# Kernel optimization log

Hardware: AMD Instinct MI355X
Metric: run time of the kernel (lower is better)

Reference implementation:

```python
import jax, jax.numpy as jnp
import numpy as np

NUM_HEADS = 4
C_IN = 80   # in_channels[0] (raw camera BEV channels)
C = 126     # in_channels[1]
D = C + 2   # 128, inner attention dim


def _conv(x, w, b=None):
    # NCHW conv, 3x3, SAME padding (padding=1)
    y = jax.lax.conv_general_dilated(x, w, (1, 1), 'SAME',
                                     dimension_numbers=('NCHW', 'OIHW', 'NCHW'))
    if b is not None:
        y = y + b[None, :, None, None]
    return y


def setup_inputs() -> dict:
    key = jax.random.key(0)
    ks = jax.random.split(key, 16)
    s = 0.02
    inp = {
        'lidar_bev': jax.random.normal(ks[0], (1, C, 64, 64), jnp.float32),
        'cam_bev': jax.random.normal(ks[1], (1, C_IN, 64, 64), jnp.float32),
        'cam_enc_w': jax.random.normal(ks[2], (C, C_IN, 3, 3), jnp.float32) * s,
        'cam_enc_b': jnp.zeros((C,), jnp.float32),
        'cam_v_w': jax.random.normal(ks[3], (D, C), jnp.float32) * s,
        'cam_qk_w': jax.random.normal(ks[4], (2 * D, C), jnp.float32) * s,
        'cam_proj_w': jax.random.normal(ks[5], (C, D), jnp.float32) * s,
        'cam_proj_b': jnp.zeros((C,), jnp.float32),
        'lidar_v_w': jax.random.normal(ks[6], (D, C), jnp.float32) * s,
        'lidar_qk_w': jax.random.normal(ks[7], (2 * D, C), jnp.float32) * s,
        'lidar_proj_w': jax.random.normal(ks[8], (C, D), jnp.float32) * s,
        'lidar_proj_b': jnp.zeros((C,), jnp.float32),
        'fuser_w': jax.random.normal(ks[9], (C, 4 * C, 3, 3), jnp.float32) * s,
    }
    return inp


def reference(lidar_bev, cam_bev, cam_enc_w, cam_enc_b, cam_v_w, cam_qk_w,
              cam_proj_w, cam_proj_b, lidar_v_w, lidar_qk_w, lidar_proj_w,
              lidar_proj_b, fuser_w):
    B, Cc, H, W = lidar_bev.shape
    N = H * W
    nh, hd = NUM_HEADS, D // NUM_HEADS
    scale = Cc ** (-0.5)  # in_channels[1] ** -0.5

    cam_enc = _conv(cam_bev, cam_enc_w, cam_enc_b)  # [B,C,H,W] (SCNET stand-in)

    cam_f = cam_enc.reshape(B, Cc, N).transpose(0, 2, 1)     # [B,N,C]
    lid_f = lidar_bev.reshape(B, Cc, N).transpose(0, 2, 1)    # [B,N,C]

    def heads(x):  # [B,N,D] -> [B,nh,N,hd]
        return x.reshape(B, N, nh, hd).transpose(0, 2, 1, 3)

    cam_v = heads(cam_f @ cam_v_w.T)
    lid_v = heads(lid_f @ lidar_v_w.T)

    def qk(x, w):  # -> (q, k) each [B,nh,N,hd]
        t = (x @ w.T).reshape(B, N, 2, nh, hd).transpose(2, 0, 3, 1, 4)
        return t[0], t[1]

    lid_q, lid_k = qk(lid_f, lidar_qk_w)
    cam_q, cam_k = qk(cam_f, cam_qk_w)

    def merge(o):  # [B,nh,N,hd] -> [B,N,D]
        return o.transpose(0, 2, 1, 3).reshape(B, N, D)

    def to_map(x):  # [B,N,C] -> [B,C,H,W]
        return x.reshape(B, H, W, Cc).transpose(0, 3, 1, 2)

    # lidar-driven attention, reused against two value tensors
    lid_attn = jax.nn.softmax(jnp.einsum('bhnd,bhmd->bhnm', lid_q, lid_k) * scale, axis=-1)
    cam_by_lid = to_map(merge(lid_attn @ cam_v) @ cam_proj_w.T + cam_proj_b)
    cam_bev_l = cam_enc + cam_by_lid
    lid_by_lid = to_map(merge(lid_attn @ lid_v) @ lidar_proj_w.T + lidar_proj_b)
    lidar_bev_l = lidar_bev + lid_by_lid

    # camera-driven attention (note: original code uses lidar_proj for BOTH outputs here)
    cam_attn = jax.nn.softmax(jnp.einsum('bhnd,bhmd->bhnm', cam_q, cam_k) * scale, axis=-1)
    cam_by_cam = to_map(merge(cam_attn @ cam_v) @ lidar_proj_w.T + lidar_proj_b)
    cam_bev_c = cam_enc + cam_by_cam
    lid_by_cam = to_map(merge(cam_attn @ lid_v) @ lidar_proj_w.T + lidar_proj_b)
    lidar_bev_c = lidar_bev + lid_by_cam

    fused_in = jnp.concatenate([cam_bev_c, cam_bev_l, lidar_bev_c, lidar_bev_l], axis=1)
    return _conv(fused_in, fuser_w)
```

## Files before the change

### kernel.cpp

```cpp
#include <hip/hip_runtime.h>
#include <hip/hip_bf16.h>

typedef unsigned short ushort_t;
using f32x4  = __attribute__((ext_vector_type(4))) float;
using bf16x8 = __attribute__((ext_vector_type(8))) short;

#define N_PIX 4096

static __device__ __forceinline__ unsigned short f2bf(float f) {
  unsigned int u = __builtin_bit_cast(unsigned int, f);
  u += 0x7FFFu + ((u >> 16) & 1u);
  return (unsigned short)(u >> 16);
}
static __device__ __forceinline__ float bf2f(unsigned int us) {
  return __builtin_bit_cast(float, us << 16);
}

typedef union {
  uint4 u4;
  unsigned long long q[2];
  bf16x8 v;
  unsigned short us[8];
} fragU;

#define LDS_U32(p) ((unsigned)(uintptr_t)((__attribute__((address_space(3))) void*)(p)))

__global__ __launch_bounds__(256) void zero_span_k(uint4* __restrict__ p, int n16) {
  int i = blockIdx.x * 256 + threadIdx.x;
  if (i < n16) p[i] = (uint4){0u, 0u, 0u, 0u};
}

__global__ __launch_bounds__(256) void pack_w_k(
    const float* __restrict__ cam_enc_w, const float* __restrict__ fuser_w,
    const float* __restrict__ lid_proj_w, const float* __restrict__ cam_proj_w,
    const float* __restrict__ lid_qk_w, const float* __restrict__ cam_qk_w,
    const float* __restrict__ cam_v_w, const float* __restrict__ lid_v_w,
    ushort_t* __restrict__ Wp_c, ushort_t* __restrict__ Wp_f,
    ushort_t* __restrict__ Wp_lid, ushort_t* __restrict__ Wp_cam,
    ushort_t* __restrict__ Wq) {
  const float QSCALE = 0.08908708063747479f * 1.4426950408889634f;
  int idx = blockIdx.x * 256 + threadIdx.x;
  if (idx < 110592) {
    int kk = idx / 12288, r = idx % 12288;
    int co = r / 96, ci = r % 96;
    float v = (co < 126 && ci < 80) ? cam_enc_w[(co * 80 + ci) * 9 + kk] : 0.f;
    Wp_c[idx] = f2bf(v);
  } else if (idx < 700416) {
    int j = idx - 110592;
    int kk = j / 65536, r = j % 65536;
    int co = r / 512, ci = r % 512;
    float v = (co < 126 && ci < 504) ? fuser_w[(co * 504 + ci) * 9 + kk] : 0.f;
    Wp_f[j] = f2bf(v);
  } else if (idx < 716800) {
    int j = idx - 700416;
    int co = j >> 7, k = j & 127;
    Wp_lid[j] = f2bf(co < 126 ? lid_proj_w[co * 128 + k] : 0.f);
  } else if (idx < 733184) {
    int j = idx - 716800;
    int co = j >> 7, k = j & 127;
    Wp_cam[j] = f2bf(co < 126 ? cam_proj_w[co * 128 + k] : 0.f);
  } else if (idx < 831488) {
    int j = idx - 733184;
    int t = j >> 14, r = j & 16383;
    int row = r >> 7, ci = r & 127;
    float v = 0.f;
    if (ci < 126) {
      if (t == 0)      v = lid_qk_w[row * 126 + ci] * QSCALE;
      else if (t == 1) v = lid_qk_w[(128 + row) * 126 + ci];
      else if (t == 2) v = cam_qk_w[row * 126 + ci] * QSCALE;
      else if (t == 3) v = cam_qk_w[(128 + row) * 126 + ci];
      else if (t == 4) v = cam_v_w[row * 126 + ci];
      else             v = lid_v_w[row * 126 + ci];
    }
    Wq[j] = f2bf(v);
  }
}

__global__ __launch_bounds__(256) void convert_in_k(
    const float* __restrict__ cam, const float* __restrict__ lidar,
    ushort_t* __restrict__ m, ushort_t* __restrict__ h,
    ushort_t* __restrict__ lidBF) {
  int idx = blockIdx.x * 256 + threadIdx.x;
  if (idx < 327680) {
    int ch = idx >> 12, n = idx & 4095;
    int y = n >> 6, x = n & 63;
    unsigned short b = f2bf(cam[idx]);
    m[ch * 4224 + (y + 1) * 64 + x] = b;
    h[ch * 4356 + (y + 1) * 66 + (x + 1)] = b;
  } else {
    int j = idx - 327680;
    if (j < 516096) lidBF[j] = f2bf(lidar[j]);
  }
}

__global__ __launch_bounds__(256) void conv_mfma_k(
    const ushort_t* __restrict__ Amain,
    const ushort_t* __restrict__ Ahalo,
    const ushort_t* __restrict__ Wp,
    ushort_t* __restrict__ parts,
    int CIp, int ksteps) {
  __shared__ __align__(16) ushort_t Abuf[2][2048];
  const int y   = blockIdx.x;
  const int kk  = blockIdx.y;
  const int ky  = kk / 3, kx = kk - ky * 3;
  const int tid = threadIdx.x;
  const int w   = tid >> 6, l = tid & 63;
  const int lane15 = l & 15, g = l >> 4;
  const int yy1 = y + ky;

  const int ci_l = w * 8 + (l >> 5) * 4 + ((l & 7) >> 1);
  const int m0   = ((l >> 3) & 3) * 16 + (l & 1) * 8;
  const ushort_t* src;
  size_t plane;
  if (kx == 1) { plane = 66 * 64; src = Amain + (size_t)ci_l * plane + yy1 * 64 + m0; }
  else         { plane = 66 * 66; src = Ahalo + (size_t)ci_l * plane + yy1 * 66 + m0 + kx; }

  const ushort_t* wbase = Wp + ((size_t)kk * 128 + w * 32 + lane15) * CIp + g * 8;
  const unsigned tr_base = LDS_U32(&Abuf[0][0]) + (unsigned)(g * 1024 + lane15 * 8);

  f32x4 acc[4][2];
  #pragma unroll
  for (int q = 0; q < 4; ++q) {
    acc[q][0] = (f32x4){0.f, 0.f, 0.f, 0.f};
    acc[q][1] = (f32x4){0.f, 0.f, 0.f, 0.f};
  }

  __builtin_amdgcn_global_load_lds(
      (const __attribute__((address_space(1))) unsigned*)src,
      (__attribute__((address_space(3))) unsigned*)(&Abuf[0][w * 512]), 16, 0, 0);
  __syncthreads();

  for (int s = 0; s < ksteps; ++s) {
    if (s + 1 < ksteps) {
      const ushort_t* srcn = src + (size_t)(s + 1) * 32 * plane;
      __builtin_amdgcn_global_load_lds(
          (const __attribute__((address_space(1))) unsigned*)srcn,
          (__attribute__((address_space(3))) unsigned*)(&Abuf[(s + 1) & 1][w * 512]), 16, 0, 0);
    }
    const ushort_t* wb = wbase + s * 32;
    fragU fb0, fb1;
    fb0.u4 = *(const uint4*)(wb);
    fb1.u4 = *(const uint4*)(wb + 16 * CIp);

    unsigned ta = tr_base + (unsigned)((s & 1) << 12);
    unsigned long long r00, r01, r10, r11, r20, r21, r30, r31;
    asm volatile("ds_read_b64_tr_b16 %0, %1 offset:0"   : "=v"(r00) : "v"(ta));
    asm volatile("ds_read_b64_tr_b16 %0, %1 offset:512" : "=v"(r01) : "v"(ta));
    asm volatile("ds_read_b64_tr_b16 %0, %1 offset:128" : "=v"(r10) : "v"(ta));
    asm volatile("ds_read_b64_tr_b16 %0, %1 offset:640" : "=v"(r11) : "v"(ta));
    asm volatile("ds_read_b64_tr_b16 %0, %1 offset:256" : "=v"(r20) : "v"(ta));
    asm volatile("ds_read_b64_tr_b16 %0, %1 offset:768" : "=v"(r21) : "v"(ta));
    asm volatile("ds_read_b64_tr_b16 %0, %1 offset:384" : "=v"(r30) : "v"(ta));
    asm volatile("ds_read_b64_tr_b16 %0, %1 offset:896" : "=v"(r31) : "v"(ta));
    asm volatile("s_waitcnt lgkmcnt(0)" ::: "memory");
    __builtin_amdgcn_sched_barrier(0);

    fragU fa;
    fa.q[0] = r00; fa.q[1] = r01;
    acc[0][0] = __builtin_amdgcn_mfma_f32_16x16x32_bf16(fa.v, fb0.v, acc[0][0], 0, 0, 0);
    acc[0][1] = __builtin_amdgcn_mfma_f32_16x16x32_bf16(fa.v, fb1.v, acc[0][1], 0, 0, 0);
    fa.q[0] = r10; fa.q[1] = r11;
    acc[1][0] = __builtin_amdgcn_mfma_f32_16x16x32_bf16(fa.v, fb0.v, acc[1][0], 0, 0, 0);
    acc[1][1] = __builtin_amdgcn_mfma_f32_16x16x32_bf16(fa.v, fb1.v, acc[1][1], 0, 0, 0);
    fa.q[0] = r20; fa.q[1] = r21;
    acc[2][0] = __builtin_amdgcn_mfma_f32_16x16x32_bf16(fa.v, fb0.v, acc[2][0], 0, 0, 0);
    acc[2][1] = __builtin_amdgcn_mfma_f32_16x16x32_bf16(fa.v, fb1.v, acc[2][1], 0, 0, 0);
    fa.q[0] = r30; fa.q[1] = r31;
    acc[3][0] = __builtin_amdgcn_mfma_f32_16x16x32_bf16(fa.v, fb0.v, acc[3][0], 0, 0, 0);
    acc[3][1] = __builtin_amdgcn_mfma_f32_16x16x32_bf16(fa.v, fb1.v, acc[3][1], 0, 0, 0);
    __syncthreads();
  }

  ushort_t* pout = parts + (size_t)kk * 524288 + (size_t)(w * 32 + lane15) * 4096
                 + y * 64 + g * 4;
  #pragma unroll
  for (int q = 0; q < 4; ++q) {
    ushort4 p0, p1;
    p0.x = f2bf(acc[q][0][0]); p0.y = f2bf(acc[q][0][1]);
    p0.z = f2bf(acc[q][0][2]); p0.w = f2bf(acc[q][0][3]);
    p1.x = f2bf(acc[q][1][0]); p1.y = f2bf(acc[q][1][1]);
    p1.z = f2bf(acc[q][1][2]); p1.w = f2bf(acc[q][1][3]);
    *(ushort4*)(pout + q * 16)             = p0;
    *(ushort4*)(pout + 16 * 4096 + q * 16) = p1;
  }
}

__global__ __launch_bounds__(256) void reduce9_k(
    const ushort_t* __restrict__ parts, float* __restrict__ out,
    ushort_t* __restrict__ outbf, const float* __restrict__ bias) {
  int n0 = (blockIdx.x * 256 + threadIdx.x) * 8;
  int co = blockIdx.y;
  size_t off = (size_t)co * 4096 + n0;
  float s[8] = {0, 0, 0, 0, 0, 0, 0, 0};
  #pragma unroll
  for (int kk = 0; kk < 9; ++kk) {
    uint4 v = *(const uint4*)(parts + (size_t)kk * 524288 + off);
    s[0] += bf2f(v.x & 0xffffu); s[1] += bf2f(v.x >> 16);
    s[2] += bf2f(v.y & 0xffffu); s[3] += bf2f(v.y >> 16);
    s[4] += bf2f(v.z & 0xffffu); s[5] += bf2f(v.z >> 16);
    s[6] += bf2f(v.w & 0xffffu); s[7] += bf2f(v.w >> 16);
  }
  float b = bias ? bias[co] : 0.f;
  #pragma unroll
  for (int i = 0; i < 8; ++i) s[i] += b;
  f32x4 o0 = {s[0], s[1], s[2], s[3]};
  f32x4 o1 = {s[4], s[5], s[6], s[7]};
  *(f32x4*)(out + off)     = o0;
  *(f32x4*)(out + off + 4) = o1;
  if (outbf) {
    ushort4 b0, b1;
    b0.x = f2bf(s[0]); b0.y = f2bf(s[1]); b0.z = f2bf(s[2]); b0.w = f2bf(s[3]);
    b1.x = f2bf(s[4]); b1.y = f2bf(s[5]); b1.z = f2bf(s[6]); b1.w = f2bf(s[7]);
    *(ushort4*)(outbf + off)     = b0;
    *(ushort4*)(outbf + off + 4) = b1;
  }
}

__global__ __launch_bounds__(256) void qkv_mfma_k(
    const ushort_t* __restrict__ lidBF, const ushort_t* __restrict__ camBF,
    const ushort_t* __restrict__ Wq,
    ushort_t* __restrict__ lidQK, ushort_t* __restrict__ camQK,
    ushort_t* __restrict__ camV, ushort_t* __restrict__ lidV) {
  __shared__ __align__(16) ushort_t Abuf[2][2048];
  const int y = blockIdx.x, t = blockIdx.y;
  const ushort_t* X = (t >= 2 && t <= 4) ? camBF : lidBF;
  const int tid = threadIdx.x;
  const int w = tid >> 6, l = tid & 63;
  const int lane15 = l & 15, g = l >> 4;
  const int ci_l = w * 8 + (l >> 5) * 4 + ((l & 7) >> 1);
  const int m0   = ((l >> 3) & 3) * 16 + (l & 1) * 8;
  const ushort_t* src = X + (size_t)ci_l * 4096 + y * 64 + m0;
  const ushort_t* wbase = Wq + (size_t)t * 16384 + (w * 32 + lane15) * 128 + g * 8;
  const unsigned tr_base = LDS_U32(&Abuf[0][0]) + (unsigned)(g * 1024 + lane15 * 8);

  f32x4 acc[4][2];
  #pragma unroll
  for (int q = 0; q < 4; ++q) {
    acc[q][0] = (f32x4){0.f, 0.f, 0.f, 0.f};
    acc[q][1] = (f32x4){0.f, 0.f, 0.f, 0.f};
  }

  __builtin_amdgcn_global_load_lds(
      (const __attribute__((address_space(1))) unsigned*)src,
      (__attribute__((address_space(3))) unsigned*)(&Abuf[0][w * 512]), 16, 0, 0);
  __syncthreads();

  for (int s = 0; s < 4; ++s) {
    if (s < 3) {
      const ushort_t* srcn = src + (size_t)(s + 1) * 32 * 4096;
      __builtin_amdgcn_global_load_lds(
          (const __attribute__((address_space(1))) unsigned*)srcn,
          (__attribute__((address_space(3))) unsigned*)(&Abuf[(s + 1) & 1][w * 512]), 16, 0, 0);
    }
    const ushort_t* wb = wbase + s * 32;
    fragU fb0, fb1;
    fb0.u4 = *(const uint4*)(wb);
    fb1.u4 = *(const uint4*)(wb + 16 * 128);

    unsigned ta = tr_base + (unsigned)((s & 1) << 12);
    unsigned long long r00, r01, r10, r11, r20, r21, r30, r31;
    asm volatile("ds_read_b64_tr_b16 %0, %1 offset:0"   : "=v"(r00) : "v"(ta));
    asm volatile("ds_read_b64_tr_b16 %0, %1 offset:512" : "=v"(r01) : "v"(ta));
    asm volatile("ds_read_b64_tr_b16 %0, %1 offset:128" : "=v"(r10) : "v"(ta));
    asm volatile("ds_read_b64_tr_b16 %0, %1 offset:640" : "=v"(r11) : "v"(ta));
    asm volatile("ds_read_b64_tr_b16 %0, %1 offset:256" : "=v"(r20) : "v"(ta));
    asm volatile("ds_read_b64_tr_b16 %0, %1 offset:768" : "=v"(r21) : "v"(ta));
    asm volatile("ds_read_b64_tr_b16 %0, %1 offset:384" : "=v"(r30) : "v"(ta));
    asm volatile("ds_read_b64_tr_b16 %0, %1 offset:896" : "=v"(r31) : "v"(ta));
    asm volatile("s_waitcnt lgkmcnt(0)" ::: "memory");
    __builtin_amdgcn_sched_barrier(0);

    fragU fa;
    fa.q[0] = r00; fa.q[1] = r01;
    acc[0][0] = __builtin_amdgcn_mfma_f32_16x16x32_bf16(fa.v, fb0.v, acc[0][0], 0, 0, 0);
    acc[0][1] = __builtin_amdgcn_mfma_f32_16x16x32_bf16(fa.v, fb1.v, acc[0][1], 0, 0, 0);
    fa.q[0] = r10; fa.q[1] = r11;
    acc[1][0] = __builtin_amdgcn_mfma_f32_16x16x32_bf16(fa.v, fb0.v, acc[1][0], 0, 0, 0);
    acc[1][1] = __builtin_amdgcn_mfma_f32_16x16x32_bf16(fa.v, fb1.v, acc[1][1], 0, 0, 0);
    fa.q[0] = r20; fa.q[1] = r21;
    acc[2][0] = __builtin_amdgcn_mfma_f32_16x16x32_bf16(fa.v, fb0.v, acc[2][0], 0, 0, 0);
    acc[2][1] = __builtin_amdgcn_mfma_f32_16x16x32_bf16(fa.v, fb1.v, acc[2][1], 0, 0, 0);
    fa.q[0] = r30; fa.q[1] = r31;
    acc[3][0] = __builtin_amdgcn_mfma_f32_16x16x32_bf16(fa.v, fb0.v, acc[3][0], 0, 0, 0);
    acc[3][1] = __builtin_amdgcn_mfma_f32_16x16x32_bf16(fa.v, fb1.v, acc[3][1], 0, 0, 0);
    __syncthreads();
  }

  if (t < 4) {
    ushort_t* dst = (t < 2) ? lidQK : camQK;
    const int colbase = (t & 1) * 128 + w * 32 + lane15;
    #pragma unroll
    for (int q = 0; q < 4; ++q)
      #pragma unroll
      for (int tt = 0; tt < 2; ++tt)
        #pragma unroll
        for (int r = 0; r < 4; ++r) {
          int n = y * 64 + q * 16 + g * 4 + r;
          dst[(size_t)n * 256 + colbase + tt * 16] = f2bf(acc[q][tt][r]);
        }
  } else {
    ushort_t* dst = (t == 4) ? camV : lidV;
    ushort_t* pout = dst + (size_t)(w * 32 + lane15) * 4096 + y * 64 + g * 4;
    #pragma unroll
    for (int q = 0; q < 4; ++q) {
      ushort4 p0, p1;
      p0.x = f2bf(acc[q][0][0]); p0.y = f2bf(acc[q][0][1]);
      p0.z = f2bf(acc[q][0][2]); p0.w = f2bf(acc[q][0][3]);
      p1.x = f2bf(acc[q][1][0]); p1.y = f2bf(acc[q][1][1]);
      p1.z = f2bf(acc[q][1][2]); p1.w = f2bf(acc[q][1][3]);
      *(ushort4*)(pout + q * 16)             = p0;
      *(ushort4*)(pout + 16 * 4096 + q * 16) = p1;
    }
  }
}

__global__ __launch_bounds__(256) void flash_attn_mfma(
    const ushort_t* __restrict__ lidQK, const ushort_t* __restrict__ camQK,
    const ushort_t* __restrict__ camV, const ushort_t* __restrict__ lidV,
    ushort_t* __restrict__ OP, float2* __restrict__ ML) {
  const int i0    = blockIdx.x * 64;
  const int h     = blockIdx.y;
  const int attn  = blockIdx.z >> 1;
  const int half  = blockIdx.z & 1;
  const int kbase = half * 2048;
  const ushort_t* QK = attn ? camQK : lidQK;

  __shared__ __align__(16) ushort_t Ks[2][64 * 40];
  __shared__ __align__(16) ushort_t Vt[2][64 * 72];
  __shared__ __align__(16) ushort_t Ps[64 * 72];

  const int tid = threadIdx.x;
  const int w = tid >> 6, l = tid & 63;
  const int m = l & 15, g = l >> 4;
  const int qrow = tid >> 2, qpart = tid & 3;
  const int vrow = tid >> 3, vj = tid & 7;
  const int vc_src = (vj - 3 * vrow) & 7;
  const int vc_sto = ((vj - vrow) & 7);

  const ushort_t* Kp = QK + (size_t)(kbase + qrow) * 256 + 128 + h * 32 + qpart * 8;
  const ushort_t* Vc = camV + (size_t)(h * 32 + (vrow & 31)) * N_PIX + kbase + vc_src * 8;
  const ushort_t* Vl = lidV + (size_t)(h * 32 + (vrow & 31)) * N_PIX + kbase + vc_src * 8;

  uint4 q4  = *(const uint4*)(QK + (size_t)(i0 + qrow) * 256 + h * 32 + qpart * 8);
  uint4 k4  = *(const uint4*)Kp;
  uint4 vc4 = *(const uint4*)Vc;
  uint4 vl4 = *(const uint4*)Vl;
  *(uint4*)(&Ps[qrow * 40 + qpart * 8]) = q4;
  __syncthreads();
  bf16x8 qfrag = *(const bf16x8*)(&Ps[(w * 16 + m) * 40 + g * 8]);
  *(uint4*)(&Ks[0][qrow * 40 + qpart * 8]) = k4;
  *(uint4*)(&Vt[0][vrow * 72 + vc_sto * 8]) = vc4;
  *(uint4*)(&Vt[0][(vrow + 32) * 72 + vc_sto * 8]) = vl4;
  __syncthreads();

  fragU ones;
  #pragma unroll
  for (int j = 0; j < 8; ++j) ones.us[j] = 0x3F80;

  f32x4 Oacc[4];
  #pragma unroll
  for (int t = 0; t < 4; ++t) Oacc[t] = (f32x4){0.f, 0.f, 0.f, 0.f};
  f32x4 lacc = (f32x4){0.f, 0.f, 0.f, 0.f};
  float mrun = -1e30f;

  const int vcs0 = ((g + 2 * m) & 7) * 8;
  const int vcs1 = ((4 + g + 2 * m) & 7) * 8;

  for (int it = 0; it < 32; ++it) {
    const int cur = it & 1, nxt = cur ^ 1;
    const bool more = (it + 1) < 32;
    uint4 kn, vcn, vln;
    if (more) {
      kn  = *(const uint4*)(Kp + (size_t)(it + 1) * 16384);
      vcn = *(const uint4*)(Vc + (it + 1) * 64);
      vln = *(const uint4*)(Vl + (it + 1) * 64);
    }

    f32x4 S[4];
    __builtin_amdgcn_s_setprio(1);
    #pragma unroll
    for (int nb = 0; nb < 4; ++nb) {
      bf16x8 kb = *(const bf16x8*)(&Ks[cur][(nb * 16 + m) * 40 + g * 8]);
      f32x4 z = (f32x4){0.f, 0.f, 0.f, 0.f};
      S[nb] = __builtin_amdgcn_mfma_f32_16x16x32_bf16(kb, qfrag, z, 0, 0, 0);
    }
    __builtin_amdgcn_s_setprio(0);

    float mx = fmaxf(fmaxf(fmaxf(S[0][0], S[0][1]), fmaxf(S[0][2], S[0][3])),
                     fmaxf(fmaxf(S[1][0], S[1][1]), fmaxf(S[1][2], S[1][3])));
    mx = fmaxf(mx, fmaxf(fmaxf(fmaxf(S[2][0], S[2][1]), fmaxf(S[2][2], S[2][3])),
                         fmaxf(fmaxf(S[3][0], S[3][1]), fmaxf(S[3][2], S[3][3]))));
    if (__any(mx > mrun + 6.f)) {
      float gm = mx;
      gm = fmaxf(gm, __shfl_xor(gm, 1));
      gm = fmaxf(gm, __shfl_xor(gm, 2));
      gm = fmaxf(gm, __shfl_xor(gm, 4));
      gm = fmaxf(gm, __shfl_xor(gm, 8));
      gm = fmaxf(gm, __shfl_xor(gm, 16));
      gm = fmaxf(gm, __shfl_xor(gm, 32));
      if (gm > mrun) {
        float corr = __builtin_amdgcn_exp2f(mrun - gm);
        #pragma unroll
        for (int t = 0; t < 4; ++t)
          #pragma unroll
          for (int r = 0; r < 4; ++r) Oacc[t][r] *= corr;
        #pragma unroll
        for (int r = 0; r < 4; ++r) lacc[r] *= corr;
        mrun = gm;
      }
    }

    #pragma unroll
    for (int nb = 0; nb < 4; ++nb)
      #pragma unroll
      for (int r = 0; r < 4; ++r)
        S[nb][r] = __builtin_amdgcn_exp2f(S[nb][r] - mrun);

    #pragma unroll
    for (int nb = 0; nb < 4; ++nb) {
      unsigned d0, d1;
      asm("v_cvt_pk_bf16_f32 %0, %1, %2" : "=v"(d0) : "v"(S[nb][0]), "v"(S[nb][1]));
      asm("v_cvt_pk_bf16_f32 %0, %1, %2" : "=v"(d1) : "v"(S[nb][2]), "v"(S[nb][3]));
      uint2 dd; dd.x = d0; dd.y = d1;
      *(uint2*)(&Ps[(w * 16 + m) * 72 + nb * 16 + g * 4]) = dd;
    }

    __builtin_amdgcn_s_setprio(1);
    #pragma unroll
    for (int ks = 0; ks < 2; ++ks) {
      bf16x8 pa = *(const bf16x8*)(&Ps[(w * 16 + m) * 72 + ks * 32 + g * 8]);
      const int vcs = ks ? vcs1 : vcs0;
      #pragma unroll
      for (int t = 0; t < 4; ++t) {
        bf16x8 vb = *(const bf16x8*)(&Vt[cur][(t * 16 + m) * 72 + vcs]);
        Oacc[t] = __builtin_amdgcn_mfma_f32_16x16x32_bf16(pa, vb, Oacc[t], 0, 0, 0);
      }
      lacc = __builtin_amdgcn_mfma_f32_16x16x32_bf16(pa, ones.v, lacc, 0, 0, 0);
    }
    __builtin_amdgcn_s_setprio(0);

    if (more) {
      *(uint4*)(&Ks[nxt][qrow * 40 + qpart * 8]) = kn;
      *(uint4*)(&Vt[nxt][vrow * 72 + vc_sto * 8]) = vcn;
      *(uint4*)(&Vt[nxt][(vrow + 32) * 72 + vc_sto * 8]) = vln;
    }
    __syncthreads();
  }

  ushort_t* OPc = OP + (size_t)((attn * 2 + half) * 2 + 0) * 4096 * 128;
  ushort_t* OPl = OP + (size_t)((attn * 2 + half) * 2 + 1) * 4096 * 128;
  #pragma unroll
  for (int t = 0; t < 4; ++t) {
    ushort_t* Ob = (t < 2) ? OPc : OPl;
    int d = h * 32 + (t & 1) * 16 + m;
    #pragma unroll
    for (int r = 0; r < 4; ++r) {
      int n = i0 + w * 16 + g * 4 + r;
      Ob[(size_t)n * 128 + d] = f2bf(Oacc[t][r]);
    }
  }
  if (m == 0) {
    #pragma unroll
    for (int r = 0; r < 4; ++r) {
      float2 v; v.x = mrun; v.y = lacc[r];
      ML[(size_t)(attn * 2 + half) * 4096 + i0 + w * 16 + g * 4 + r] = v;
    }
  }
}

__global__ __launch_bounds__(256) void proj_mfma_k(
    const ushort_t* __restrict__ OP, const float2* __restrict__ ML,
    const ushort_t* __restrict__ Wlid, const ushort_t* __restrict__ Wcam,
    const float* __restrict__ cam_enc, const float* __restrict__ lidar_bev,
    const float* __restrict__ cam_proj_b, const float* __restrict__ lid_proj_b,
    ushort_t* __restrict__ fm, ushort_t* __restrict__ fh) {
  const int n0 = blockIdx.x * 64;
  const int ot = blockIdx.y;
  const int attn = (ot == 0 || ot == 2) ? 1 : 0;
  const int vt = ot >> 1;
  const int tid = threadIdx.x;
  const int w = tid >> 6, l = tid & 63;
  const int m = l & 15, g = l >> 4;

  const ushort_t* Oa = OP + (size_t)((attn * 2 + 0) * 2 + vt) * 4096 * 128;
  const ushort_t* Ob = OP + (size_t)((attn * 2 + 1) * 2 + vt) * 4096 * 128;
  const float2* MLa = ML + (size_t)(attn * 2 + 0) * 4096;
  const float2* MLb = ML + (size_t)(attn * 2 + 1) * 4096;

  const int arow = n0 + w * 16 + m;
  float2 mla = MLa[arow], mlb = MLb[arow];
  float M  = fmaxf(mla.x, mlb.x);
  float wa = __builtin_amdgcn_exp2f(mla.x - M);
  float wb = __builtin_amdgcn_exp2f(mlb.x - M);
  float dn = wa * mla.y + wb * mlb.y;
  float aa = wa / dn, ab = wb / dn;

  fragU afr[4];
  #pragma unroll
  for (int s = 0; s < 4; ++s) {
    fragU xa, xb;
    xa.u4 = *(const uint4*)(Oa + (size_t)arow * 128 + s * 32 + g * 8);
    xb.u4 = *(const uint4*)(Ob + (size_t)arow * 128 + s * 32 + g * 8);
    #pragma unroll
    for (int j = 0; j < 8; ++j)
      afr[s].us[j] = f2bf(aa * bf2f(xa.us[j]) + ab * bf2f(xb.us[j]));
  }

  const ushort_t* W = (ot == 1) ? Wcam : Wlid;
  f32x4 acc[8];
  #pragma unroll
  for (int t = 0; t < 8; ++t) acc[t] = (f32x4){0.f, 0.f, 0.f, 0.f};
  #pragma unroll
  for (int s = 0; s < 4; ++s) {
    #pragma unroll
    for (int t = 0; t < 8; ++t) {
      fragU bfr;
      bfr.u4 = *(const uint4*)(W + (size_t)(t * 16 + m) * 128 + s * 32 + g * 8);
      acc[t] = __builtin_amdgcn_mfma_f32_16x16x32_bf16(afr[s].v, bfr.v, acc[t], 0, 0, 0);
    }
  }

  const float* res  = (ot < 2) ? cam_enc : lidar_bev;
  const float* bias = (ot == 1) ? cam_proj_b : lid_proj_b;
  const int doff = ot * 126;
  #pragma unroll
  for (int t = 0; t < 8; ++t) {
    int co = t * 16 + m;
    if (co < 126) {
      float b = bias[co];
      #pragma unroll
      for (int r = 0; r < 4; ++r) {
        int n = n0 + w * 16 + g * 4 + r;
        float v = acc[t][r] + res[(size_t)co * N_PIX + n] + b;
        unsigned short bf = f2bf(v);
        int y = n >> 6, x = n & 63;
        fm[(doff + co) * 4224 + (y + 1) * 64 + x]      = bf;
        fh[(doff + co) * 4356 + (y + 1) * 66 + x + 1]  = bf;
      }
    }
  }
}

extern "C" void kernel_launch(void* const* d_in, const int* in_sizes, int n_in,
                              void* d_out, int out_size, void* d_ws, size_t ws_size,
                              hipStream_t stream) {
  (void)in_sizes; (void)n_in; (void)out_size; (void)ws_size;
  const float* lidar_bev  = (const float*)d_in[0];
  const float* cam_bev    = (const float*)d_in[1];
  const float* cam_enc_w  = (const float*)d_in[2];
  const float* cam_enc_b  = (const float*)d_in[3];
  const float* cam_v_w    = (const float*)d_in[4];
  const float* cam_qk_w   = (const float*)d_in[5];
  const float* cam_proj_w = (const float*)d_in[6];
  const float* cam_proj_b = (const float*)d_in[7];
  const float* lid_v_w    = (const float*)d_in[8];
  const float* lid_qk_w   = (const float*)d_in[9];
  const float* lid_proj_w = (const float*)d_in[10];
  const float* lid_proj_b = (const float*)d_in[11];
  const float* fuser_w    = (const float*)d_in[12];
  float* out = (float*)d_out;

  char* p = (char*)d_ws;
  ushort_t* arena = (ushort_t*)p;
  ushort_t* OP    = (ushort_t*)p;
  float2*   ML    = (float2*)(p + 8388608);
  ushort_t* lidQK = (ushort_t*)(p + 9437184);
  ushort_t* camQK = (ushort_t*)(p + 11534336);
  ushort_t* camV  = (ushort_t*)(p + 13631488);
  ushort_t* lidV  = (ushort_t*)(p + 14680064);
  float*    cam_enc = (float*)(p + 15728640);
  ushort_t* Wp_c    = (ushort_t*)(p + 17793024);
  ushort_t* Wp_f    = (ushort_t*)(p + 18014208);
  ushort_t* Wp_lid  = (ushort_t*)(p + 19193856);
  ushort_t* Wp_cam  = (ushort_t*)(p + 19226624);
  ushort_t* Wq      = (ushort_t*)(p + 19259392);
  ushort_t* lidBF   = (ushort_t*)(p + 19456000);
  ushort_t* camBF   = (ushort_t*)(p + 20504576);
  ushort_t* camBF_m = (ushort_t*)(p + 21553152);
  ushort_t* camBF_h = (ushort_t*)(p + 22364160);
  ushort_t* fusBF_m = (ushort_t*)(p + 23200512);
  ushort_t* fusBF_h = (ushort_t*)(p + 27525888);

  zero_span_k<<<2548, 256, 0, stream>>>((uint4*)(p + 21553152), 652080);
  pack_w_k<<<3248, 256, 0, stream>>>(cam_enc_w, fuser_w, lid_proj_w, cam_proj_w,
                                     lid_qk_w, cam_qk_w, cam_v_w, lid_v_w,
                                     Wp_c, Wp_f, Wp_lid, Wp_cam, Wq);
  convert_in_k<<<3296, 256, 0, stream>>>(cam_bev, lidar_bev, camBF_m, camBF_h, lidBF);

  conv_mfma_k<<<dim3(64, 9), 256, 0, stream>>>(camBF_m, camBF_h, Wp_c, arena, 96, 3);
  reduce9_k<<<dim3(2, 126), 256, 0, stream>>>(arena, cam_enc, camBF, cam_enc_b);

  qkv_mfma_k<<<dim3(64, 6), 256, 0, stream>>>(lidBF, camBF, Wq, lidQK, camQK, camV, lidV);
  flash_attn_mfma<<<dim3(64, 4, 4), 256, 0, stream>>>(lidQK, camQK, camV, lidV, OP, ML);
  proj_mfma_k<<<dim3(64, 4), 256, 0, stream>>>(OP, ML, Wp_lid, Wp_cam, cam_enc, lidar_bev,
                                               cam_proj_b, lid_proj_b, fusBF_m, fusBF_h);

  conv_mfma_k<<<dim3(64, 9), 256, 0, stream>>>(fusBF_m, fusBF_h, Wp_f, arena, 512, 16);
  reduce9_k<<<dim3(2, 126), 256, 0, stream>>>(arena, out, nullptr, nullptr);
}
```

Baseline: 128.2 us.

## Rewrite flash attention with 32x32 MFMA and register-resident P via permlane swaps

The attention kernel moves from 16x16x32 to 32x32x16 bf16 MFMA tiles. Each wave now handles 32 query rows, so a block covers 128 queries and the grid is halved. The softmax probabilities are repacked in registers with permlane32_swap instead of going through an LDS P buffer, which removes that LDS round trip. The row sum is computed with VALU adds and a shuffle rather than an extra MFMA against a ones vector. In exchange there are more accumulator registers per wave, which may lower occupancy, and only 512 blocks are launched.

Result: faster. 117.2 us (-8.6%).

```diff
diff --git a/kernel.cpp b/kernel.cpp
--- a/kernel.cpp
+++ b/kernel.cpp
@@ -3,7 +3,9 @@
 
 typedef unsigned short ushort_t;
 using f32x4  = __attribute__((ext_vector_type(4))) float;
+using f32x16 = __attribute__((ext_vector_type(16))) float;
 using bf16x8 = __attribute__((ext_vector_type(8))) short;
+typedef unsigned uint2v __attribute__((ext_vector_type(2)));
 
 #define N_PIX 4096
 
@@ -18,6 +20,7 @@
 
 typedef union {
   uint4 u4;
+  unsigned u[4];
   unsigned long long q[2];
   bf16x8 v;
   unsigned short us[8];
@@ -318,7 +321,7 @@
     const ushort_t* __restrict__ lidQK, const ushort_t* __restrict__ camQK,
     const ushort_t* __restrict__ camV, const ushort_t* __restrict__ lidV,
     ushort_t* __restrict__ OP, float2* __restrict__ ML) {
-  const int i0    = blockIdx.x * 64;
+  const int i0    = blockIdx.x * 128;
   const int h     = blockIdx.y;
   const int attn  = blockIdx.z >> 1;
   const int half  = blockIdx.z & 1;
@@ -327,69 +330,63 @@
 
   __shared__ __align__(16) ushort_t Ks[2][64 * 40];
   __shared__ __align__(16) ushort_t Vt[2][64 * 72];
-  __shared__ __align__(16) ushort_t Ps[64 * 72];
 
   const int tid = threadIdx.x;
   const int w = tid >> 6, l = tid & 63;
-  const int m = l & 15, g = l >> 4;
-  const int qrow = tid >> 2, qpart = tid & 3;
-  const int vrow = tid >> 3, vj = tid & 7;
-  const int vc_src = (vj - 3 * vrow) & 7;
-  const int vc_sto = ((vj - vrow) & 7);
-
-  const ushort_t* Kp = QK + (size_t)(kbase + qrow) * 256 + 128 + h * 32 + qpart * 8;
-  const ushort_t* Vc = camV + (size_t)(h * 32 + (vrow & 31)) * N_PIX + kbase + vc_src * 8;
-  const ushort_t* Vl = lidV + (size_t)(h * 32 + (vrow & 31)) * N_PIX + kbase + vc_src * 8;
-
-  uint4 q4  = *(const uint4*)(QK + (size_t)(i0 + qrow) * 256 + h * 32 + qpart * 8);
-  uint4 k4  = *(const uint4*)Kp;
-  uint4 vc4 = *(const uint4*)Vc;
-  uint4 vl4 = *(const uint4*)Vl;
-  *(uint4*)(&Ps[qrow * 40 + qpart * 8]) = q4;
+  const int q31 = l & 31, hi = l >> 5;
+  const int q0w = i0 + w * 32;
+
+  const int srow = tid >> 2, sc = tid & 3;
+  const ushort_t* Kg = QK + (size_t)(kbase + srow) * 256 + 128 + h * 32 + sc * 8;
+  const ushort_t* Vg = ((srow >> 5) ? lidV : camV)
+                     + (size_t)(h * 32 + (srow & 31)) * N_PIX + kbase;
+
+  fragU qf0, qf1;
+  qf0.u4 = *(const uint4*)(QK + (size_t)(q0w + q31) * 256 + h * 32 + hi * 8);
+  qf1.u4 = *(const uint4*)(QK + (size_t)(q0w + q31) * 256 + h * 32 + 16 + hi * 8);
+
+  {
+    uint4 k4 = *(const uint4*)Kg;
+    uint4 va = *(const uint4*)(Vg + sc * 8);
+    uint4 vb = *(const uint4*)(Vg + (sc + 4) * 8);
+    *(uint4*)(&Ks[0][srow * 40 + sc * 8]) = k4;
+    *(uint4*)(&Vt[0][srow * 72 + sc * 8]) = va;
+    *(uint4*)(&Vt[0][srow * 72 + (sc + 4) * 8]) = vb;
+  }
   __syncthreads();
-  bf16x8 qfrag = *(const bf16x8*)(&Ps[(w * 16 + m) * 40 + g * 8]);
-  *(uint4*)(&Ks[0][qrow * 40 + qpart * 8]) = k4;
-  *(uint4*)(&Vt[0][vrow * 72 + vc_sto * 8]) = vc4;
-  *(uint4*)(&Vt[0][(vrow + 32) * 72 + vc_sto * 8]) = vl4;
-  __syncthreads();
-
-  fragU ones;
-  #pragma unroll
-  for (int j = 0; j < 8; ++j) ones.us[j] = 0x3F80;
-
-  f32x4 Oacc[4];
-  #pragma unroll
-  for (int t = 0; t < 4; ++t) Oacc[t] = (f32x4){0.f, 0.f, 0.f, 0.f};
-  f32x4 lacc = (f32x4){0.f, 0.f, 0.f, 0.f};
-  float mrun = -1e30f;
-
-  const int vcs0 = ((g + 2 * m) & 7) * 8;
-  const int vcs1 = ((4 + g + 2 * m) & 7) * 8;
+
+  f32x16 Oc = (f32x16)0.f, Ol = (f32x16)0.f;
+  float lrun = 0.f, mrun = -1e30f;
 
   for (int it = 0; it < 32; ++it) {
     const int cur = it & 1, nxt = cur ^ 1;
     const bool more = (it + 1) < 32;
-    uint4 kn, vcn, vln;
+    uint4 kn, van, vbn;
     if (more) {
-      kn  = *(const uint4*)(Kp + (size_t)(it + 1) * 16384);
-      vcn = *(const uint4*)(Vc + (it + 1) * 64);
-      vln = *(const uint4*)(Vl + (it + 1) * 64);
-    }
-
-    f32x4 S[4];
+      kn  = *(const uint4*)(Kg + (size_t)(it + 1) * 16384);
+      van = *(const uint4*)(Vg + (it + 1) * 64 + sc * 8);
+      vbn = *(const uint4*)(Vg + (it + 1) * 64 + (sc + 4) * 8);
+    }
+
+    const ushort_t* kb = &Ks[cur][0];
+    fragU k00, k01, k10, k11;
+    k00.u4 = *(const uint4*)(kb + q31 * 40 + hi * 8);
+    k01.u4 = *(const uint4*)(kb + q31 * 40 + 16 + hi * 8);
+    k10.u4 = *(const uint4*)(kb + (32 + q31) * 40 + hi * 8);
+    k11.u4 = *(const uint4*)(kb + (32 + q31) * 40 + 16 + hi * 8);
+    f32x16 S0, S1;
     __builtin_amdgcn_s_setprio(1);
-    #pragma unroll
-    for (int nb = 0; nb < 4; ++nb) {
-      bf16x8 kb = *(const bf16x8*)(&Ks[cur][(nb * 16 + m) * 40 + g * 8]);
-      f32x4 z = (f32x4){0.f, 0.f, 0.f, 0.f};
-      S[nb] = __builtin_amdgcn_mfma_f32_16x16x32_bf16(kb, qfrag, z, 0, 0, 0);
-    }
+    S0 = __builtin_amdgcn_mfma_f32_32x32x16_bf16(k00.v, qf0.v, (f32x16)0.f, 0, 0, 0);
+    S0 = __builtin_amdgcn_mfma_f32_32x32x16_bf16(k01.v, qf1.v, S0, 0, 0, 0);
+    S1 = __builtin_amdgcn_mfma_f32_32x32x16_bf16(k10.v, qf0.v, (f32x16)0.f, 0, 0, 0);
+    S1 = __builtin_amdgcn_mfma_f32_32x32x16_bf16(k11.v, qf1.v, S1, 0, 0, 0);
     __builtin_amdgcn_s_setprio(0);
 
-    float mx = fmaxf(fmaxf(fmaxf(S[0][0], S[0][1]), fmaxf(S[0][2], S[0][3])),
-                     fmaxf(fmaxf(S[1][0], S[1][1]), fmaxf(S[1][2], S[1][3])));
-    mx = fmaxf(mx, fmaxf(fmaxf(fmaxf(S[2][0], S[2][1]), fmaxf(S[2][2], S[2][3])),
-                         fmaxf(fmaxf(S[3][0], S[3][1]), fmaxf(S[3][2], S[3][3]))));
+    float mx = S0[0];
+    #pragma unroll
+    for (int j = 1; j < 16; ++j) mx = fmaxf(mx, S0[j]);
+    #pragma unroll
+    for (int j = 0; j < 16; ++j) mx = fmaxf(mx, S1[j]);
     if (__any(mx > mrun + 6.f)) {
       float gm = mx;
       gm = fmaxf(gm, __shfl_xor(gm, 1));
@@ -400,71 +397,102 @@
       gm = fmaxf(gm, __shfl_xor(gm, 32));
       if (gm > mrun) {
         float corr = __builtin_amdgcn_exp2f(mrun - gm);
-        #pragma unroll
-        for (int t = 0; t < 4; ++t)
-          #pragma unroll
-          for (int r = 0; r < 4; ++r) Oacc[t][r] *= corr;
-        #pragma unroll
-        for (int r = 0; r < 4; ++r) lacc[r] *= corr;
+        Oc = Oc * corr;
+        Ol = Ol * corr;
+        lrun *= corr;
         mrun = gm;
       }
     }
-
-    #pragma unroll
-    for (int nb = 0; nb < 4; ++nb)
-      #pragma unroll
-      for (int r = 0; r < 4; ++r)
-        S[nb][r] = __builtin_amdgcn_exp2f(S[nb][r] - mrun);
-
-    #pragma unroll
-    for (int nb = 0; nb < 4; ++nb) {
-      unsigned d0, d1;
-      asm("v_cvt_pk_bf16_f32 %0, %1, %2" : "=v"(d0) : "v"(S[nb][0]), "v"(S[nb][1]));
-      asm("v_cvt_pk_bf16_f32 %0, %1, %2" : "=v"(d1) : "v"(S[nb][2]), "v"(S[nb][3]));
-      uint2 dd; dd.x = d0; dd.y = d1;
-      *(uint2*)(&Ps[(w * 16 + m) * 72 + nb * 16 + g * 4]) = dd;
-    }
-
+    float ps = 0.f;
+    #pragma unroll
+    for (int j = 0; j < 16; ++j) {
+      float p = __builtin_amdgcn_exp2f(S0[j] - mrun);
+      S0[j] = p; ps += p;
+    }
+    #pragma unroll
+    for (int j = 0; j < 16; ++j) {
+      float p = __builtin_amdgcn_exp2f(S1[j] - mrun);
+      S1[j] = p; ps += p;
+    }
+    ps += __shfl_xor(ps, 32);
+    lrun += ps;
+
+    fragU pa0, pa1, pa2, pa3;
+    {
+      unsigned a0, a1, b0, b1;
+      asm("v_cvt_pk_bf16_f32 %0, %1, %2" : "=v"(a0) : "v"(S0[0]),  "v"(S0[1]));
+      asm("v_cvt_pk_bf16_f32 %0, %1, %2" : "=v"(a1) : "v"(S0[2]),  "v"(S0[3]));
+      asm("v_cvt_pk_bf16_f32 %0, %1, %2" : "=v"(b0) : "v"(S0[4]),  "v"(S0[5]));
+      asm("v_cvt_pk_bf16_f32 %0, %1, %2" : "=v"(b1) : "v"(S0[6]),  "v"(S0[7]));
+      uint2v r0 = __builtin_amdgcn_permlane32_swap(a0, b0, false, false);
+      uint2v r1 = __builtin_amdgcn_permlane32_swap(a1, b1, false, false);
+      pa0.u[0] = r0[0]; pa0.u[1] = r1[0]; pa0.u[2] = r0[1]; pa0.u[3] = r1[1];
+      asm("v_cvt_pk_bf16_f32 %0, %1, %2" : "=v"(a0) : "v"(S0[8]),  "v"(S0[9]));
+      asm("v_cvt_pk_bf16_f32 %0, %1, %2" : "=v"(a1) : "v"(S0[10]), "v"(S0[11]));
+      asm("v_cvt_pk_bf16_f32 %0, %1, %2" : "=v"(b0) : "v"(S0[12]), "v"(S0[13]));
+      asm("v_cvt_pk_bf16_f32 %0, %1, %2" : "=v"(b1) : "v"(S0[14]), "v"(S0[15]));
+      r0 = __builtin_amdgcn_permlane32_swap(a0, b0, false, false);
+      r1 = __builtin_amdgcn_permlane32_swap(a1, b1, false, false);
+      pa1.u[0] = r0[0]; pa1.u[1] = r1[0]; pa1.u[2] = r0[1]; pa1.u[3] = r1[1];
+      asm("v_cvt_pk_bf16_f32 %0, %1, %2" : "=v"(a0) : "v"(S1[0]),  "v"(S1[1]));
+      asm("v_cvt_pk_bf16_f32 %0, %1, %2" : "=v"(a1) : "v"(S1[2]),  "v"(S1[3]));
+      asm("v_cvt_pk_bf16_f32 %0, %1, %2" : "=v"(b0) : "v"(S1[4]),  "v"(S1[5]));
+      asm("v_cvt_pk_bf16_f32 %0, %1, %2" : "=v"(b1) : "v"(S1[6]),  "v"(S1[7]));
+      r0 = __builtin_amdgcn_permlane32_swap(a0, b0, false, false);
+      r1 = __builtin_amdgcn_permlane32_swap(a1, b1, false, false);
+      pa2.u[0] = r0[0]; pa2.u[1] = r1[0]; pa2.u[2] = r0[1]; pa2.u[3] = r1[1];
+      asm("v_cvt_pk_bf16_f32 %0, %1, %2" : "=v"(a0) : "v"(S1[8]),  "v"(S1[9]));
+      asm("v_cvt_pk_bf16_f32 %0, %1, %2" : "=v"(a1) : "v"(S1[10]), "v"(S1[11]));
+      asm("v_cvt_pk_bf16_f32 %0, %1, %2" : "=v"(b0) : "v"(S1[12]), "v"(S1[13]));
+      asm("v_cvt_pk_bf16_f32 %0, %1, %2" : "=v"(b1) : "v"(S1[14]), "v"(S1[15]));
+      r0 = __builtin_amdgcn_permlane32_swap(a0, b0, false, false);
+      r1 = __builtin_amdgcn_permlane32_swap(a1, b1, false, false);
+      pa3.u[0] = r0[0]; pa3.u[1] = r1[0]; pa3.u[2] = r0[1]; pa3.u[3] = r1[1];
+    }
+
+    const ushort_t* vb = &Vt[cur][0];
     __builtin_amdgcn_s_setprio(1);
-    #pragma unroll
-    for (int ks = 0; ks < 2; ++ks) {
-      bf16x8 pa = *(const bf16x8*)(&Ps[(w * 16 + m) * 72 + ks * 32 + g * 8]);
-      const int vcs = ks ? vcs1 : vcs0;
-      #pragma unroll
-      for (int t = 0; t < 4; ++t) {
-        bf16x8 vb = *(const bf16x8*)(&Vt[cur][(t * 16 + m) * 72 + vcs]);
-        Oacc[t] = __builtin_amdgcn_mfma_f32_16x16x32_bf16(pa, vb, Oacc[t], 0, 0, 0);
-      }
-      lacc = __builtin_amdgcn_mfma_f32_16x16x32_bf16(pa, ones.v, lacc, 0, 0, 0);
+    {
+      fragU vc, vl;
+      vc.u4 = *(const uint4*)(vb + q31 * 72 + hi * 8);
+      vl.u4 = *(const uint4*)(vb + (32 + q31) * 72 + hi * 8);
+      Oc = __builtin_amdgcn_mfma_f32_32x32x16_bf16(pa0.v, vc.v, Oc, 0, 0, 0);
+      Ol = __builtin_amdgcn_mfma_f32_32x32x16_bf16(pa0.v, vl.v, Ol, 0, 0, 0);
+      vc.u4 = *(const uint4*)(vb + q31 * 72 + 16 + hi * 8);
+      vl.u4 = *(const uint4*)(vb + (32 + q31) * 72 + 16 + hi * 8);
+      Oc = __builtin_amdgcn_mfma_f32_32x32x16_bf16(pa1.v, vc.v, Oc, 0, 0, 0);
+      Ol = __builtin_amdgcn_mfma_f32_32x32x16_bf16(pa1.v, vl.v, Ol, 0, 0, 0);
+      vc.u4 = *(const uint4*)(vb + q31 * 72 + 32 + hi * 8);
+      vl.u4 = *(const uint4*)(vb + (32 + q31) * 72 + 32 + hi * 8);
+      Oc = __builtin_amdgcn_mfma_f32_32x32x16_bf16(pa2.v, vc.v, Oc, 0, 0, 0);
+      Ol = __builtin_amdgcn_mfma_f32_32x32x16_bf16(pa2.v, vl.v, Ol, 0, 0, 0);
+      vc.u4 = *(const uint4*)(vb + q31 * 72 + 48 + hi * 8);
+      vl.u4 = *(const uint4*)(vb + (32 + q31) * 72 + 48 + hi * 8);
+      Oc = __builtin_amdgcn_mfma_f32_32x32x16_bf16(pa3.v, vc.v, Oc, 0, 0, 0);
+      Ol = __builtin_amdgcn_mfma_f32_32x32x16_bf16(pa3.v, vl.v, Ol, 0, 0, 0);
     }
     __builtin_amdgcn_s_setprio(0);
 
     if (more) {
-      *(uint4*)(&Ks[nxt][qrow * 40 + qpart * 8]) = kn;
-      *(uint4*)(&Vt[nxt][vrow * 72 + vc_sto * 8]) = vcn;
-      *(uint4*)(&Vt[nxt][(vrow + 32) * 72 + vc_sto * 8]) = vln;
+      *(uint4*)(&Ks[nxt][srow * 40 + sc * 8]) = kn;
+      *(uint4*)(&Vt[nxt][srow * 72 + sc * 8]) = van;
+      *(uint4*)(&Vt[nxt][srow * 72 + (sc + 4) * 8]) = vbn;
     }
     __syncthreads();
   }
 
   ushort_t* OPc = OP + (size_t)((attn * 2 + half) * 2 + 0) * 4096 * 128;
   ushort_t* OPl = OP + (size_t)((attn * 2 + half) * 2 + 1) * 4096 * 128;
-  #pragma unroll
-  for (int t = 0; t < 4; ++t) {
-    ushort_t* Ob = (t < 2) ? OPc : OPl;
-    int d = h * 32 + (t & 1) * 16 + m;
-    #pragma unroll
-    for (int r = 0; r < 4; ++r) {
-      int n = i0 + w * 16 + g * 4 + r;
-      Ob[(size_t)n * 128 + d] = f2bf(Oacc[t][r]);
-    }
-  }
-  if (m == 0) {
-    #pragma unroll
-    for (int r = 0; r < 4; ++r) {
-      float2 v; v.x = mrun; v.y = lacc[r];
-      ML[(size_t)(attn * 2 + half) * 4096 + i0 + w * 16 + g * 4 + r] = v;
-    }
+  const int d = h * 32 + q31;
+  #pragma unroll
+  for (int reg = 0; reg < 16; ++reg) {
+    int n = q0w + (reg & 3) + 8 * (reg >> 2) + 4 * hi;
+    OPc[(size_t)n * 128 + d] = f2bf(Oc[reg]);
+    OPl[(size_t)n * 128 + d] = f2bf(Ol[reg]);
+  }
+  if (l < 32) {
+    float2 v; v.x = mrun; v.y = lrun;
+    ML[(size_t)(attn * 2 + half) * 4096 + q0w + l] = v;
   }
 }
 
@@ -591,7 +619,7 @@
   reduce9_k<<<dim3(2, 126), 256, 0, stream>>>(arena, cam_enc, camBF, cam_enc_b);
 
   qkv_mfma_k<<<dim3(64, 6), 256, 0, stream>>>(lidBF, camBF, Wq, lidQK, camQK, camV, lidV);
-  flash_attn_mfma<<<dim3(64, 4, 4), 256, 0, stream>>>(lidQK, camQK, camV, lidV, OP, ML);
+  flash_attn_mfma<<<dim3(32, 4, 4), 256, 0, stream>>>(lidQK, camQK, camV, lidV, OP, ML);
   proj_mfma_k<<<dim3(64, 4), 256, 0, stream>>>(OP, ML, Wp_lid, Wp_cam, cam_enc, lidar_bev,
                                                cam_proj_b, lid_proj_b, fusBF_m, fusBF_h);
 
```
